# Optimization experiments

Hardware: AMD Instinct MI355X
Metric: run time of the kernel (lower is better)

Reference implementation:

```python
import jax, jax.numpy as jnp
import numpy as np

N = 8192


def setup_inputs() -> dict:
    key = jax.random.key(0)
    ks = jax.random.split(key, 12)
    H_emb = jax.random.normal(ks[0], (645, 1140), jnp.float32) * 0.05
    H_emb = H_emb.at[0].set(0.0)  # padding_idx=0
    inp = {
        "ld_gcn": jax.random.normal(ks[1], (N, 512), jnp.float32),
        "ld_encoder": jax.random.normal(ks[2], (N, 512), jnp.float32),
        "x": jax.random.randint(ks[3], (N,), 0, 240),
        "y": jax.random.randint(ks[4], (N,), 0, 404),
        "H_emb": H_emb,
        "conv_w": jax.random.normal(ks[5], (32, 1, 2, 25), jnp.float32) * (1.0 / np.sqrt(2 * 25)),
        "conv_b": jnp.zeros((32,), jnp.float32),
        "W1": jax.random.normal(ks[6], (1000, 3968), jnp.float32) * (1.0 / np.sqrt(3968)),
        "b1": jnp.zeros((1000,), jnp.float32),
        "W2": jax.random.normal(ks[7], (100, 1000), jnp.float32) * (1.0 / np.sqrt(1000)),
        "b2": jnp.zeros((100,), jnp.float32),
        "Wg": jax.random.normal(ks[8], (100, 512), jnp.float32) * (1.0 / np.sqrt(512)),
        "bg": jnp.zeros((100,), jnp.float32),
        "We": jax.random.normal(ks[9], (100, 512), jnp.float32) * (1.0 / np.sqrt(512)),
        "be": jnp.zeros((100,), jnp.float32),
    }
    return inp


def reference(ld_gcn, ld_encoder, x, y, H_emb, conv_w, conv_b, W1, b1, W2, b2, Wg, bg, We, be):
    n = x.shape[0]
    lrelu = lambda t: jax.nn.leaky_relu(t, 0.01)
    # embedding lookups + concat -> (n,1,2,1140)
    h = jnp.concatenate([H_emb[x], H_emb[y + 240]], axis=1).reshape(n, 1, 2, 1140)
    # CNN: conv (2,25) stride (1,9) valid -> (n,32,1,124)
    c = jax.lax.conv_general_dilated(h, conv_w, window_strides=(1, 9), padding="VALID",
                                     dimension_numbers=("NCHW", "OIHW", "NCHW"))
    c = lrelu(c + conv_b[None, :, None, None]).reshape(n, -1)  # (n,3968)
    # fc_H (dropout = identity at eval)
    hfc = lrelu(c @ W1.T + b1)
    hfc = lrelu(hfc @ W2.T + b2)  # (n,100)
    # gating projections
    g = jnp.tanh(ld_gcn @ Wg.T + bg)       # (n,100)
    e = jnp.tanh(ld_encoder @ We.T + be)   # (n,100)
    # diagonal of (n,100)@(100,n) == row-wise dot product
    a_gcn = jnp.einsum("nd,nd->n", g, hfc)
    a_enc = jnp.einsum("nd,nd->n", e, hfc)
    att = jax.nn.softmax(jnp.stack([a_gcn, a_enc], axis=1), axis=1)  # (n,2)
    return ld_gcn * att[:, :1], ld_encoder * att[:, 1:]
```

## Files before the change

### kernel.cpp

```cpp
#include <hip/hip_runtime.h>
#include <hip/hip_bf16.h>

typedef unsigned short u16;
typedef short bf16x8 __attribute__((ext_vector_type(8)));
typedef float f32x4 __attribute__((ext_vector_type(4)));

#define NROWS 8192
#define EMBD  1140
#define FDIM  3968
#define N1R   1000
#define N1P   1024
#define N2R   100
#define N2P   128
#define DG    512

__device__ inline u16 f2b(float f) {
  __hip_bfloat16 h = __float2bfloat16(f);
  return *reinterpret_cast<u16*>(&h);
}

__device__ inline float tanh_fast(float x) {
  float ax = fabsf(x);
  float t = __expf(-2.f * ax);
  float r = (1.f - t) / (1.f + t);
  return x < 0.f ? -r : r;
}

__device__ inline void gld16(const void* g, void* l) {
  __builtin_amdgcn_global_load_lds(
      (const __attribute__((address_space(1))) unsigned int*)g,
      (__attribute__((address_space(3))) unsigned int*)l, 16, 0, 0);
}

__global__ __launch_bounds__(256) void prep_kernel(
    const float* __restrict__ W1, const float* __restrict__ W2,
    const float* __restrict__ Wg, const float* __restrict__ We,
    const float* __restrict__ H_emb, const float* __restrict__ conv_w,
    const float* __restrict__ conv_b,
    u16* __restrict__ W1bf, u16* __restrict__ W2bf,
    u16* __restrict__ Wgbf, u16* __restrict__ Webf,
    float* __restrict__ Abuf, float* __restrict__ Bbuf) {
  const int b = blockIdx.x;
  const int t = threadIdx.x;
  if (b < 2112) {
    const float* src;
    u16* dst;
    int row, c8, realRow, realCol;
    if (b < 1984) {
      int id = b * 256 + t;
      row = id / 496; c8 = (id - row * 496) * 8;
      src = W1 + (size_t)row * FDIM + c8;
      dst = W1bf + (size_t)row * FDIM + c8;
      realRow = N1R; realCol = FDIM;
    } else if (b < 2048) {
      int id = (b - 1984) * 256 + t;
      row = id >> 7; c8 = (id & 127) * 8;
      src = W2 + (size_t)row * N1R + c8;
      dst = W2bf + (size_t)row * N1P + c8;
      realRow = N2R; realCol = N1R;
    } else if (b < 2080) {
      int id = (b - 2048) * 256 + t;
      row = id >> 6; c8 = (id & 63) * 8;
      src = Wg + (size_t)row * DG + c8;
      dst = Wgbf + (size_t)row * DG + c8;
      realRow = N2R; realCol = DG;
    } else {
      int id = (b - 2080) * 256 + t;
      row = id >> 6; c8 = (id & 63) * 8;
      src = We + (size_t)row * DG + c8;
      dst = Webf + (size_t)row * DG + c8;
      realRow = N2R; realCol = DG;
    }
    bf16x8 o = (bf16x8){0, 0, 0, 0, 0, 0, 0, 0};
    if (row < realRow && c8 < realCol) {
#pragma unroll
      for (int j = 0; j < 8; ++j) o[j] = (short)f2b(src[j]);
    }
    *(bf16x8*)dst = o;
    return;
  }
  __shared__ float se[EMBD];
  __shared__ float sw[32 * 25];
  __shared__ float sb[32];
  const int eb = b - 2112;
  bool isA = eb < 240;
  const float* emb = H_emb + (size_t)eb * EMBD;
  float* outp = isA ? (Abuf + (size_t)eb * FDIM) : (Bbuf + (size_t)(eb - 240) * FDIM);
  for (int i = t; i < EMBD; i += 256) se[i] = emb[i];
  int kh = isA ? 0 : 1;
  for (int i = t; i < 800; i += 256) {
    int o = i / 25, kw = i - o * 25;
    sw[i] = conv_w[o * 50 + kh * 25 + kw];
  }
  if (t < 32) sb[t] = isA ? conv_b[t] : 0.f;
  __syncthreads();
  for (int f = t; f < FDIM; f += 256) {
    int o = f / 124, wpos = f - o * 124;
    const float* e = se + wpos * 9;
    const float* wp = sw + o * 25;
    float acc = sb[o];
#pragma unroll
    for (int kw = 0; kw < 25; ++kw) acc += wp[kw] * e[kw];
    outp[f] = acc;
  }
}

__global__ __launch_bounds__(256) void conv_combine_kernel(
    const float* __restrict__ Abuf, const float* __restrict__ Bbuf,
    const int* __restrict__ xi, const int* __restrict__ yi, u16* __restrict__ cbf) {
  int r = blockIdx.x;
  const float4* pa = (const float4*)(Abuf + (size_t)xi[r] * FDIM);
  const float4* pb = (const float4*)(Bbuf + (size_t)yi[r] * FDIM);
  u16* out = cbf + (size_t)r * FDIM;
  for (int i = threadIdx.x; i < FDIM / 4; i += 256) {
    float4 a = pa[i], b = pb[i];
    float v0 = a.x + b.x, v1 = a.y + b.y, v2 = a.z + b.z, v3 = a.w + b.w;
    v0 = v0 > 0.f ? v0 : 0.01f * v0;
    v1 = v1 > 0.f ? v1 : 0.01f * v1;
    v2 = v2 > 0.f ? v2 : 0.01f * v2;
    v3 = v3 > 0.f ? v3 : 0.01f * v3;
    ushort4 o;
    o.x = f2b(v0); o.y = f2b(v1); o.z = f2b(v2); o.w = f2b(v3);
    *(ushort4*)(out + i * 4) = o;
  }
}

__global__ __launch_bounds__(256) void fc1_kernel(
    const u16* __restrict__ A, const u16* __restrict__ B,
    const float* __restrict__ bias, int realN,
    u16* __restrict__ C, int K, int ldc, int nTilesX) {
  const int nwg = gridDim.x;
  const int cpx = nwg >> 3;
  const int bid = blockIdx.x;
  const int wg = (bid & 7) * cpx + (bid >> 3);
  const int tm = (wg / nTilesX) * 128;
  const int tn = (wg % nTilesX) * 128;

  __shared__ u16 As[2][8192];
  __shared__ u16 Bs[2][8192];
  const int t = threadIdx.x;
  const int lane = t & 63;
  const int w = t >> 6;
  const int wr = (w >> 1) * 64, wc = (w & 1) * 64;
  const int fr = lane & 15;
  const int kg = lane >> 4;

  const int srow = lane >> 3;
  const int su = ((lane & 7) ^ srow) * 8;
  const u16* gA[4];
  const u16* gB[4];
  int ldsOff[4];
#pragma unroll
  for (int i = 0; i < 4; ++i) {
    const int c = w + i * 4;
    gA[i] = A + (size_t)(tm + c * 8 + srow) * K + su;
    gB[i] = B + (size_t)(tn + c * 8 + srow) * K + su;
    ldsOff[i] = c * 512;
  }

  f32x4 acc[4][4];
#pragma unroll
  for (int m = 0; m < 4; ++m)
#pragma unroll
    for (int n = 0; n < 4; ++n) acc[m][n] = (f32x4){0.f, 0.f, 0.f, 0.f};

  const int nk = K >> 6;
#pragma unroll
  for (int i = 0; i < 4; ++i) {
    gld16(gA[i], &As[0][ldsOff[i]]);
    gld16(gB[i], &Bs[0][ldsOff[i]]);
  }
  __syncthreads();

  for (int kt = 0; kt < nk; ++kt) {
    const int cb = kt & 1;
    if (kt + 1 < nk) {
      const int ko = (kt + 1) << 6;
#pragma unroll
      for (int i = 0; i < 4; ++i) {
        gld16(gA[i] + ko, &As[cb ^ 1][ldsOff[i]]);
        gld16(gB[i] + ko, &Bs[cb ^ 1][ldsOff[i]]);
      }
    }
    __builtin_amdgcn_sched_barrier(0);
#pragma unroll
    for (int ks = 0; ks < 2; ++ks) {
      const int un = ((ks * 4 + kg) ^ (fr & 7)) << 4;
      bf16x8 af[4], bff[4];
#pragma unroll
      for (int m = 0; m < 4; ++m)
        af[m] = *(const bf16x8*)((const char*)As[cb] + (wr + m * 16 + fr) * 128 + un);
#pragma unroll
      for (int n = 0; n < 4; ++n)
        bff[n] = *(const bf16x8*)((const char*)Bs[cb] + (wc + n * 16 + fr) * 128 + un);
#pragma unroll
      for (int m = 0; m < 4; ++m)
#pragma unroll
        for (int n = 0; n < 4; ++n)
          acc[m][n] = __builtin_amdgcn_mfma_f32_16x16x32_bf16(af[m], bff[n], acc[m][n], 0, 0, 0);
    }
    __syncthreads();
  }

#pragma unroll
  for (int n = 0; n < 4; ++n) {
    int col = tn + wc + n * 16 + fr;
    float bv = (col < realN) ? bias[col] : 0.f;
#pragma unroll
    for (int m = 0; m < 4; ++m) {
#pragma unroll
      for (int j = 0; j < 4; ++j) {
        int row = tm + wr + m * 16 + kg * 4 + j;
        float v = acc[m][n][j] + bv;
        v = v > 0.f ? v : 0.01f * v;
        C[(size_t)row * ldc + col] = f2b(v);
      }
    }
  }
}

__global__ __launch_bounds__(256) void tail_kernel(
    const u16* __restrict__ hfc1, const u16* __restrict__ W2bf, const float* __restrict__ b2,
    const float* __restrict__ ldg, const float* __restrict__ lde,
    const u16* __restrict__ Wgbf, const float* __restrict__ bg,
    const u16* __restrict__ Webf, const float* __restrict__ be,
    float* __restrict__ out0, float* __restrict__ out1) {
  __shared__ float H16[N2P][16];
  __shared__ float dpart[2][4][16];
  __shared__ float wt[2][16];

  const int tm = blockIdx.x * 16;
  const int t = threadIdx.x;
  const int lane = t & 63;
  const int w = t >> 6;
  const int fr = lane & 15;
  const int kg = lane >> 4;
  const int n0 = w * 2;

  {
    f32x4 a0 = (f32x4){0.f, 0.f, 0.f, 0.f}, a1 = a0;
    const u16* Ap = hfc1 + (size_t)(tm + fr) * N1P + kg * 8;
    const u16* B0 = W2bf + (size_t)(n0 * 16 + fr) * N1P + kg * 8;
    const u16* B1 = B0 + (size_t)16 * N1P;
#pragma unroll 8
    for (int kt = 0; kt < N1P / 32; ++kt) {
      bf16x8 af = *(const bf16x8*)(Ap + kt * 32);
      bf16x8 f0 = *(const bf16x8*)(B0 + kt * 32);
      bf16x8 f1 = *(const bf16x8*)(B1 + kt * 32);
      a0 = __builtin_amdgcn_mfma_f32_16x16x32_bf16(af, f0, a0, 0, 0, 0);
      a1 = __builtin_amdgcn_mfma_f32_16x16x32_bf16(af, f1, a1, 0, 0, 0);
    }
#pragma unroll
    for (int n = 0; n < 2; ++n) {
      int col = (n0 + n) * 16 + fr;
      float bv = (col < N2R) ? b2[col] : 0.f;
      f32x4 v = n == 0 ? a0 : a1;
      f32x4 o;
#pragma unroll
      for (int j = 0; j < 4; ++j) {
        float x = v[j] + bv;
        o[j] = x > 0.f ? x : 0.01f * x;
      }
      *(f32x4*)&H16[col][kg * 4] = o;
    }
  }
  __syncthreads();

#pragma unroll 1
  for (int sec = 0; sec < 2; ++sec) {
    const float* ld = sec == 0 ? ldg : lde;
    const u16* Wb = sec == 0 ? Wgbf : Webf;
    const float* bb = sec == 0 ? bg : be;

    f32x4 a0 = (f32x4){0.f, 0.f, 0.f, 0.f}, a1 = a0;
    const float* Ap = ld + (size_t)(tm + fr) * DG + kg * 8;
    const u16* B0 = Wb + (size_t)(n0 * 16 + fr) * DG + kg * 8;
    const u16* B1 = B0 + (size_t)16 * DG;
#pragma unroll 4
    for (int kt = 0; kt < DG / 32; ++kt) {
      float4 v0 = *(const float4*)(Ap + kt * 32);
      float4 v1 = *(const float4*)(Ap + kt * 32 + 4);
      bf16x8 af;
      af[0] = (short)f2b(v0.x); af[1] = (short)f2b(v0.y);
      af[2] = (short)f2b(v0.z); af[3] = (short)f2b(v0.w);
      af[4] = (short)f2b(v1.x); af[5] = (short)f2b(v1.y);
      af[6] = (short)f2b(v1.z); af[7] = (short)f2b(v1.w);
      bf16x8 f0 = *(const bf16x8*)(B0 + kt * 32);
      bf16x8 f1 = *(const bf16x8*)(B1 + kt * 32);
      a0 = __builtin_amdgcn_mfma_f32_16x16x32_bf16(af, f0, a0, 0, 0, 0);
      a1 = __builtin_amdgcn_mfma_f32_16x16x32_bf16(af, f1, a1, 0, 0, 0);
    }
    float dv[4] = {0.f, 0.f, 0.f, 0.f};
#pragma unroll
    for (int n = 0; n < 2; ++n) {
      int col = (n0 + n) * 16 + fr;
      float bv = (col < N2R) ? bb[col] : 0.f;
      f32x4 v = n == 0 ? a0 : a1;
      f32x4 h = *(const f32x4*)&H16[col][kg * 4];
#pragma unroll
      for (int j = 0; j < 4; ++j)
        dv[j] += tanh_fast(v[j] + bv) * h[j];
    }
#pragma unroll
    for (int j = 0; j < 4; ++j) {
      float v = dv[j];
      v += __shfl_xor(v, 1);
      v += __shfl_xor(v, 2);
      v += __shfl_xor(v, 4);
      v += __shfl_xor(v, 8);
      dv[j] = v;
    }
    if (fr == 0) {
#pragma unroll
      for (int j = 0; j < 4; ++j) dpart[sec][w][kg * 4 + j] = dv[j];
    }
  }
  __syncthreads();

  if (t < 16) {
    float ag = dpart[0][0][t] + dpart[0][1][t] + dpart[0][2][t] + dpart[0][3][t];
    float ae = dpart[1][0][t] + dpart[1][1][t] + dpart[1][2][t] + dpart[1][3][t];
    float mm = fmaxf(ag, ae);
    float eg = __expf(ag - mm), eo = __expf(ae - mm);
    float inv = 1.f / (eg + eo);
    wt[0][t] = eg * inv;
    wt[1][t] = eo * inv;
  }
  __syncthreads();

  for (int i = t; i < 16 * (DG / 4); i += 256) {
    int r = i >> 7, c = i & 127;
    float w0 = wt[0][r], w1 = wt[1][r];
    size_t off = (size_t)(tm + r) * DG + c * 4;
    float4 a = *(const float4*)(ldg + off);
    a.x *= w0; a.y *= w0; a.z *= w0; a.w *= w0;
    *(float4*)(out0 + off) = a;
    float4 b = *(const float4*)(lde + off);
    b.x *= w1; b.y *= w1; b.z *= w1; b.w *= w1;
    *(float4*)(out1 + off) = b;
  }
}

extern "C" void kernel_launch(void* const* d_in, const int* in_sizes, int n_in,
                              void* d_out, int out_size, void* d_ws, size_t ws_size,
                              hipStream_t stream) {
  const float* ld_gcn = (const float*)d_in[0];
  const float* ld_enc = (const float*)d_in[1];
  const int*   xi     = (const int*)d_in[2];
  const int*   yi     = (const int*)d_in[3];
  const float* H_emb  = (const float*)d_in[4];
  const float* conv_w = (const float*)d_in[5];
  const float* conv_b = (const float*)d_in[6];
  const float* W1     = (const float*)d_in[7];
  const float* b1     = (const float*)d_in[8];
  const float* W2     = (const float*)d_in[9];
  const float* b2     = (const float*)d_in[10];
  const float* Wg     = (const float*)d_in[11];
  const float* bg     = (const float*)d_in[12];
  const float* We     = (const float*)d_in[13];
  const float* be     = (const float*)d_in[14];

  char* ws = (char*)d_ws;
  size_t off = 0;
  auto alloc = [&](size_t bytes) -> void* {
    void* p = ws + off;
    off = (off + bytes + 255) & ~(size_t)255;
    return p;
  };
  float* Abuf = (float*)alloc(240ull * FDIM * 4);
  float* Bbuf = (float*)alloc(404ull * FDIM * 4);
  u16*   cbf  = (u16*)  alloc((size_t)NROWS * FDIM * 2);
  u16*   W1bf = (u16*)  alloc((size_t)N1P * FDIM * 2);
  u16*   W2bf = (u16*)  alloc((size_t)N2P * N1P * 2);
  u16*   Wgbf = (u16*)  alloc((size_t)N2P * DG * 2);
  u16*   Webf = (u16*)  alloc((size_t)N2P * DG * 2);
  u16*   hfc1 = (u16*)  alloc((size_t)NROWS * N1P * 2);
  if (ws_size < off) return;

  prep_kernel<<<2756, 256, 0, stream>>>(W1, W2, Wg, We, H_emb, conv_w, conv_b,
                                        W1bf, W2bf, Wgbf, Webf, Abuf, Bbuf);
  conv_combine_kernel<<<NROWS, 256, 0, stream>>>(Abuf, Bbuf, xi, yi, cbf);

  fc1_kernel<<<dim3((NROWS / 128) * (N1P / 128)), 256, 0, stream>>>(
      cbf, W1bf, b1, N1R, hfc1, FDIM, N1P, N1P / 128);

  float* out0 = (float*)d_out;
  float* out1 = out0 + (size_t)NROWS * DG;
  tail_kernel<<<NROWS / 16, 256, 0, stream>>>(
      hfc1, W2bf, b2, ld_gcn, ld_enc, Wgbf, bg, Webf, be, out0, out1);
}
```

Before: 196.6 us.

## Store conv partials in bf16 and deepen fc1 prefetch to two stages

Conv partial sums Abuf/Bbuf are now stored as bf16 instead of fp32, halving the gather traffic in conv_combine, which reads them with 16-byte vector loads. The fc1 GEMM loop is restructured to issue global-to-LDS loads two k-tiles ahead, with explicit vmcnt waits and raw barriers instead of __syncthreads, so load latency overlaps more MFMA work. The bf16 partials add an extra rounding step before the sum and leaky ReLU, which slightly reduces accuracy.

```diff
diff --git a/kernel.cpp b/kernel.cpp
--- a/kernel.cpp
+++ b/kernel.cpp
@@ -19,6 +19,13 @@
   return *reinterpret_cast<u16*>(&h);
 }
 
+__device__ inline float b2f(u16 u) {
+  unsigned v = (unsigned)u << 16;
+  union { unsigned u; float f; } c;
+  c.u = v;
+  return c.f;
+}
+
 __device__ inline float tanh_fast(float x) {
   float ax = fabsf(x);
   float t = __expf(-2.f * ax);
@@ -39,7 +46,7 @@
     const float* __restrict__ conv_b,
     u16* __restrict__ W1bf, u16* __restrict__ W2bf,
     u16* __restrict__ Wgbf, u16* __restrict__ Webf,
-    float* __restrict__ Abuf, float* __restrict__ Bbuf) {
+    u16* __restrict__ Abuf, u16* __restrict__ Bbuf) {
   const int b = blockIdx.x;
   const int t = threadIdx.x;
   if (b < 2112) {
@@ -85,7 +92,7 @@
   const int eb = b - 2112;
   bool isA = eb < 240;
   const float* emb = H_emb + (size_t)eb * EMBD;
-  float* outp = isA ? (Abuf + (size_t)eb * FDIM) : (Bbuf + (size_t)(eb - 240) * FDIM);
+  u16* outp = isA ? (Abuf + (size_t)eb * FDIM) : (Bbuf + (size_t)(eb - 240) * FDIM);
   for (int i = t; i < EMBD; i += 256) se[i] = emb[i];
   int kh = isA ? 0 : 1;
   for (int i = t; i < 800; i += 256) {
@@ -101,27 +108,27 @@
     float acc = sb[o];
 #pragma unroll
     for (int kw = 0; kw < 25; ++kw) acc += wp[kw] * e[kw];
-    outp[f] = acc;
+    outp[f] = f2b(acc);
   }
 }
 
 __global__ __launch_bounds__(256) void conv_combine_kernel(
-    const float* __restrict__ Abuf, const float* __restrict__ Bbuf,
+    const u16* __restrict__ Abuf, const u16* __restrict__ Bbuf,
     const int* __restrict__ xi, const int* __restrict__ yi, u16* __restrict__ cbf) {
   int r = blockIdx.x;
-  const float4* pa = (const float4*)(Abuf + (size_t)xi[r] * FDIM);
-  const float4* pb = (const float4*)(Bbuf + (size_t)yi[r] * FDIM);
-  u16* out = cbf + (size_t)r * FDIM;
-  for (int i = threadIdx.x; i < FDIM / 4; i += 256) {
-    float4 a = pa[i], b = pb[i];
-    float v0 = a.x + b.x, v1 = a.y + b.y, v2 = a.z + b.z, v3 = a.w + b.w;
-    v0 = v0 > 0.f ? v0 : 0.01f * v0;
-    v1 = v1 > 0.f ? v1 : 0.01f * v1;
-    v2 = v2 > 0.f ? v2 : 0.01f * v2;
-    v3 = v3 > 0.f ? v3 : 0.01f * v3;
-    ushort4 o;
-    o.x = f2b(v0); o.y = f2b(v1); o.z = f2b(v2); o.w = f2b(v3);
-    *(ushort4*)(out + i * 4) = o;
+  const bf16x8* pa = (const bf16x8*)(Abuf + (size_t)xi[r] * FDIM);
+  const bf16x8* pb = (const bf16x8*)(Bbuf + (size_t)yi[r] * FDIM);
+  bf16x8* out = (bf16x8*)(cbf + (size_t)r * FDIM);
+  for (int i = threadIdx.x; i < FDIM / 8; i += 256) {
+    bf16x8 a = pa[i], b = pb[i];
+    bf16x8 o;
+#pragma unroll
+    for (int j = 0; j < 8; ++j) {
+      float v = b2f((u16)a[j]) + b2f((u16)b[j]);
+      v = v > 0.f ? v : 0.01f * v;
+      o[j] = (short)f2b(v);
+    }
+    out[i] = o;
   }
 }
 
@@ -158,6 +165,14 @@
     ldsOff[i] = c * 512;
   }
 
+#define STAGE(kt_, cb_) do { \
+    const int ko_ = (kt_) << 6; \
+    _Pragma("unroll") for (int i = 0; i < 4; ++i) { \
+      gld16(gA[i] + ko_, &As[cb_][ldsOff[i]]); \
+      gld16(gB[i] + ko_, &Bs[cb_][ldsOff[i]]); \
+    } \
+  } while (0)
+
   f32x4 acc[4][4];
 #pragma unroll
   for (int m = 0; m < 4; ++m)
@@ -165,24 +180,15 @@
     for (int n = 0; n < 4; ++n) acc[m][n] = (f32x4){0.f, 0.f, 0.f, 0.f};
 
   const int nk = K >> 6;
-#pragma unroll
-  for (int i = 0; i < 4; ++i) {
-    gld16(gA[i], &As[0][ldsOff[i]]);
-    gld16(gB[i], &Bs[0][ldsOff[i]]);
-  }
-  __syncthreads();
+  STAGE(0, 0);
+  STAGE(1, 1);
+  asm volatile("s_waitcnt vmcnt(8)" ::: "memory");
+  __builtin_amdgcn_sched_barrier(0);
+  __builtin_amdgcn_s_barrier();
+  __builtin_amdgcn_sched_barrier(0);
 
   for (int kt = 0; kt < nk; ++kt) {
     const int cb = kt & 1;
-    if (kt + 1 < nk) {
-      const int ko = (kt + 1) << 6;
-#pragma unroll
-      for (int i = 0; i < 4; ++i) {
-        gld16(gA[i] + ko, &As[cb ^ 1][ldsOff[i]]);
-        gld16(gB[i] + ko, &Bs[cb ^ 1][ldsOff[i]]);
-      }
-    }
-    __builtin_amdgcn_sched_barrier(0);
 #pragma unroll
     for (int ks = 0; ks < 2; ++ks) {
       const int un = ((ks * 4 + kg) ^ (fr & 7)) << 4;
@@ -199,8 +205,20 @@
         for (int n = 0; n < 4; ++n)
           acc[m][n] = __builtin_amdgcn_mfma_f32_16x16x32_bf16(af[m], bff[n], acc[m][n], 0, 0, 0);
     }
-    __syncthreads();
-  }
+    if (kt + 1 == nk) break;
+    __builtin_amdgcn_s_barrier();
+    __builtin_amdgcn_sched_barrier(0);
+    if (kt + 2 < nk) {
+      STAGE(kt + 2, cb);
+      asm volatile("s_waitcnt vmcnt(8)" ::: "memory");
+    } else {
+      asm volatile("s_waitcnt vmcnt(0)" ::: "memory");
+    }
+    __builtin_amdgcn_sched_barrier(0);
+    __builtin_amdgcn_s_barrier();
+    __builtin_amdgcn_sched_barrier(0);
+  }
+#undef STAGE
 
 #pragma unroll
   for (int n = 0; n < 4; ++n) {
@@ -367,14 +385,14 @@
     off = (off + bytes + 255) & ~(size_t)255;
     return p;
   };
-  float* Abuf = (float*)alloc(240ull * FDIM * 4);
-  float* Bbuf = (float*)alloc(404ull * FDIM * 4);
-  u16*   cbf  = (u16*)  alloc((size_t)NROWS * FDIM * 2);
-  u16*   W1bf = (u16*)  alloc((size_t)N1P * FDIM * 2);
-  u16*   W2bf = (u16*)  alloc((size_t)N2P * N1P * 2);
-  u16*   Wgbf = (u16*)  alloc((size_t)N2P * DG * 2);
-  u16*   Webf = (u16*)  alloc((size_t)N2P * DG * 2);
-  u16*   hfc1 = (u16*)  alloc((size_t)NROWS * N1P * 2);
+  u16* Abuf = (u16*)alloc(240ull * FDIM * 2);
+  u16* Bbuf = (u16*)alloc(404ull * FDIM * 2);
+  u16* cbf  = (u16*)alloc((size_t)NROWS * FDIM * 2);
+  u16* W1bf = (u16*)alloc((size_t)N1P * FDIM * 2);
+  u16* W2bf = (u16*)alloc((size_t)N2P * N1P * 2);
+  u16* Wgbf = (u16*)alloc((size_t)N2P * DG * 2);
+  u16* Webf = (u16*)alloc((size_t)N2P * DG * 2);
+  u16* hfc1 = (u16*)alloc((size_t)NROWS * N1P * 2);
   if (ws_size < off) return;
 
   prep_kernel<<<2756, 256, 0, stream>>>(W1, W2, Wg, We, H_emb, conv_w, conv_b,
```

After: 189.6 us. -3.5%, faster.
